# Kernel tuning notes

Hardware: AMD Instinct MI355X
Metric: run time of the kernel (lower is better)

Reference implementation:

```python
import jax, jax.numpy as jnp
import numpy as np

B, C, H_RES, W_RES = 8, 192, 64, 64


def dwconv(x, kern, pad):
    # depthwise conv, x: (B,C,H,W), kern: (C,1,k,k)
    return jax.lax.conv_general_dilated(
        x, kern, window_strides=(1, 1), padding=[(pad, pad), (pad, pad)],
        dimension_numbers=('NCHW', 'OIHW', 'NCHW'),
        feature_group_count=x.shape[1])


def omni_shift(x, alpha, dw1, dw3, dw5):
    # OmniShift (training branch): learnable mix of identity + depthwise 1x1/3x3/5x5
    return (alpha[0] * x + alpha[1] * dwconv(x, dw1, 0)
            + alpha[2] * dwconv(x, dw3, 1) + alpha[3] * dwconv(x, dw5, 2))


def biwkv(w, u, k, v):
    # Bidirectional WKV (Vision-RWKV style):
    # out_t = (sum_{i!=t} e^{-(|t-i|-1)w + k_i} v_i + e^{u+k_t} v_t)
    #       / (sum_{i!=t} e^{-(|t-i|-1)w + k_i}       + e^{u+k_t})
    # w,u: (C,); k,v: (B,T,C). Implemented as two stable log-scaled scans.
    kT = jnp.moveaxis(k, 1, 0)  # (T,B,C)
    vT = jnp.moveaxis(v, 1, 0)
    bc = (k.shape[0], k.shape[2])
    init = (jnp.full(bc, -jnp.inf, k.dtype), jnp.zeros(bc, k.dtype), jnp.zeros(bc, k.dtype))

    def step(carry, inp):
        p, num, den = carry          # state = e^p * (num, den) over strictly-previous tokens
        kt, vt = inp
        out = (p, num, den)          # emit BEFORE absorbing token t (i != t term)
        q = jnp.maximum(p - w, kt)
        e1 = jnp.exp(p - w - q)
        e2 = jnp.exp(kt - q)
        return (q, e1 * num + e2 * vt, e1 * den + e2), out

    _, (pf, nf, df) = jax.lax.scan(step, init, (kT, vT))
    _, (pb, nb, db) = jax.lax.scan(step, init, (kT[::-1], vT[::-1]))
    pb, nb, db = pb[::-1], nb[::-1], db[::-1]

    ps = u + kT                      # self term exponent
    r = jnp.maximum(jnp.maximum(pf, pb), ps)
    ef, eb, es = jnp.exp(pf - r), jnp.exp(pb - r), jnp.exp(ps - r)
    out = (ef * nf + eb * nb + es * vT) / (ef * df + eb * db + es)
    return jnp.moveaxis(out, 0, 1)   # (B,T,C)


def setup_inputs() -> dict:
    key = jax.random.key(0)
    ks = jax.random.split(key, 12)
    s = 1.0 / np.sqrt(C)
    inp = {
        'x': jax.random.normal(ks[0], (B, C, H_RES, W_RES), jnp.float32),
        'w_key': jax.random.normal(ks[1], (C, C), jnp.float32) * s,
        'w_value': jax.random.normal(ks[2], (C, C), jnp.float32) * s,
        'w_recept': jax.random.normal(ks[3], (C, C), jnp.float32) * s,
        'w_out': jax.random.normal(ks[4], (C, C), jnp.float32) * s,
        'decay': jax.random.normal(ks[5], (C,), jnp.float32),
        'boost': jax.random.normal(ks[6], (C,), jnp.float32),
        'alpha': jax.random.normal(ks[7], (4,), jnp.float32),
        'dw1': jax.random.normal(ks[8], (C, 1, 1, 1), jnp.float32) * s,
        'dw3': jax.random.normal(ks[9], (C, 1, 3, 3), jnp.float32) * (s / 3.0),
        'dw5': jax.random.normal(ks[10], (C, 1, 5, 5), jnp.float32) * (s / 5.0),
        'H': H_RES,
        'W': W_RES,
    }
    return inp


def reference(x, w_key, w_value, w_recept, w_out, decay, boost, alpha, dw1, dw3, dw5, H, W):
    Bn, Cn = x.shape[0], x.shape[1]
    T = H * W
    xs = omni_shift(x, alpha, dw1, dw3, dw5)                 # (B,C,H,W)
    xt = jnp.transpose(xs.reshape(Bn, Cn, T), (0, 2, 1))     # (B,T,C)
    k = jnp.einsum('btc,dc->btd', xt, w_key)
    v = jnp.einsum('btc,dc->btd', xt, w_value)
    sr = jax.nn.sigmoid(jnp.einsum('btc,dc->btd', xt, w_recept))
    y = biwkv(decay / T, boost / T, k, v)                    # (B,T,C)
    y = sr * y
    y = jnp.einsum('btd,cd->btc', y, w_out)
    return jnp.transpose(y, (0, 2, 1)).reshape(Bn, Cn, H, W)
```

## Files before the change

kernel.cpp:

```cpp
#include <hip/hip_runtime.h>
#include <math.h>

#define Cn 192
#define Bn 8
#define Tn 4096
#define HW 64

typedef unsigned short u16;
typedef unsigned int u32;
typedef __attribute__((ext_vector_type(8))) __bf16 bf16x8;
typedef __attribute__((ext_vector_type(16))) float f32x16;

__device__ __forceinline__ void gload16(const void* g, void* l) {
    __builtin_amdgcn_global_load_lds(
        (const __attribute__((address_space(1))) void*)g,
        (__attribute__((address_space(3))) void*)l, 16, 0, 0);
}

__device__ __forceinline__ void split_bf16(float x, u16 &h, u16 &l) {
    u32 u = __float_as_uint(x);
    u32 uh = (u + 0x7FFFu + ((u >> 16) & 1u)) & 0xFFFF0000u;
    h = (u16)(uh >> 16);
    float r = x - __uint_as_float(uh);
    u32 ur = __float_as_uint(r);
    l = (u16)((ur + 0x7FFFu + ((ur >> 16) & 1u)) >> 16);
}

__global__ __launch_bounds__(256) void wsplit_kernel(const float* __restrict__ Wk,
                                                     const float* __restrict__ Wv,
                                                     const float* __restrict__ Wr,
                                                     const float* __restrict__ Wo,
                                                     u16* __restrict__ wh,
                                                     u16* __restrict__ wl) {
    const int idx = blockIdx.x * 256 + threadIdx.x;
    const int mat = blockIdx.y;
    const float* src = (mat == 0) ? Wk : (mat == 1) ? Wv : (mat == 2) ? Wr : Wo;
    u16 h, l;
    split_bf16(src[idx], h, l);
    wh[(size_t)mat * 36864 + idx] = h;
    wl[(size_t)mat * 36864 + idx] = l;
}

__global__ __launch_bounds__(256) void omni_kernel(const float* __restrict__ x,
                                                   const float* __restrict__ alpha,
                                                   const float* __restrict__ dw1,
                                                   const float* __restrict__ dw3,
                                                   const float* __restrict__ dw5,
                                                   u16* __restrict__ xhi,
                                                   u16* __restrict__ xlo) {
    const int plane = blockIdx.x;
    const int c = plane % Cn;
    const float* xin = x + (size_t)plane * Tn;
    u16* oh = xhi + (size_t)plane * Tn;
    u16* ol = xlo + (size_t)plane * Tn;

    __shared__ float tile[68 * 68];
    __shared__ float wk[25];

    const int tid = threadIdx.x;
    if (tid == 0) {
        const float a0 = alpha[0], a1 = alpha[1], a2 = alpha[2], a3 = alpha[3];
        #pragma unroll
        for (int j = 0; j < 25; ++j) wk[j] = a3 * dw5[c * 25 + j];
        #pragma unroll
        for (int dy = 0; dy < 3; ++dy)
            #pragma unroll
            for (int dx = 0; dx < 3; ++dx)
                wk[(dy + 1) * 5 + (dx + 1)] += a2 * dw3[c * 9 + dy * 3 + dx];
        wk[12] += a1 * dw1[c] + a0;
    }
    for (int i = tid; i < 68 * 68; i += 256) {
        int r = i / 68, cc = i - r * 68;
        int gy = r - 2, gx = cc - 2;
        float v = 0.f;
        if (gy >= 0 && gy < HW && gx >= 0 && gx < HW) v = xin[gy * HW + gx];
        tile[i] = v;
    }
    __syncthreads();

    const int py = tid >> 3;
    const int px0 = (tid & 7) << 3;

    #pragma unroll
    for (int half = 0; half < 2; ++half) {
        const int y = py + half * 32;
        float row[5][12];
        #pragma unroll
        for (int dy = 0; dy < 5; ++dy) {
            const float4* rp = (const float4*)&tile[(y + dy) * 68 + px0];
            float4 r0 = rp[0], r1 = rp[1], r2 = rp[2];
            row[dy][0] = r0.x; row[dy][1] = r0.y; row[dy][2]  = r0.z; row[dy][3]  = r0.w;
            row[dy][4] = r1.x; row[dy][5] = r1.y; row[dy][6]  = r1.z; row[dy][7]  = r1.w;
            row[dy][8] = r2.x; row[dy][9] = r2.y; row[dy][10] = r2.z; row[dy][11] = r2.w;
        }
        u32 ph[4], pl[4];
        #pragma unroll
        for (int jj = 0; jj < 8; ++jj) {
            float acc = 0.f;
            #pragma unroll
            for (int dy = 0; dy < 5; ++dy)
                #pragma unroll
                for (int dx = 0; dx < 5; ++dx)
                    acc = fmaf(row[dy][jj + dx], wk[dy * 5 + dx], acc);
            u16 h, l2;
            split_bf16(acc, h, l2);
            if (jj & 1) { ph[jj >> 1] |= ((u32)h) << 16; pl[jj >> 1] |= ((u32)l2) << 16; }
            else        { ph[jj >> 1] = h;               pl[jj >> 1] = l2; }
        }
        *(uint4*)&oh[y * 64 + px0] = make_uint4(ph[0], ph[1], ph[2], ph[3]);
        *(uint4*)&ol[y * 64 + px0] = make_uint4(pl[0], pl[1], pl[2], pl[3]);
    }
}

__global__ __launch_bounds__(256) void transpose_kernel(const u16* __restrict__ ih,
                                                        const u16* __restrict__ il,
                                                        u16* __restrict__ oh,
                                                        u16* __restrict__ ol) {
    __shared__ u32 T[2][128][21];
    const int tid = threadIdx.x;
    const size_t ib = (size_t)blockIdx.z * Cn * Tn;
    const int c0 = blockIdx.y * 32, t0 = blockIdx.x * 128;

    {
        const int c2 = tid >> 4;
        const int tc = (tid & 15) * 8;
        const size_t ge = ib + (size_t)(c0 + 2 * c2) * Tn + t0 + tc;
        uint4 evh = *(const uint4*)&ih[ge];
        uint4 odh = *(const uint4*)&ih[ge + Tn];
        uint4 evl = *(const uint4*)&il[ge];
        uint4 odl = *(const uint4*)&il[ge + Tn];
        const u32 eh4[4] = {evh.x, evh.y, evh.z, evh.w};
        const u32 oh4[4] = {odh.x, odh.y, odh.z, odh.w};
        const u32 el4[4] = {evl.x, evl.y, evl.z, evl.w};
        const u32 ol4[4] = {odl.x, odl.y, odl.z, odl.w};
        #pragma unroll
        for (int q = 0; q < 4; ++q) {
            T[0][tc + 2 * q    ][c2] = (eh4[q] & 0xFFFFu) | (oh4[q] << 16);
            T[0][tc + 2 * q + 1][c2] = (eh4[q] >> 16) | (oh4[q] & 0xFFFF0000u);
            T[1][tc + 2 * q    ][c2] = (el4[q] & 0xFFFFu) | (ol4[q] << 16);
            T[1][tc + 2 * q + 1][c2] = (el4[q] >> 16) | (ol4[q] & 0xFFFF0000u);
        }
    }
    __syncthreads();
    {
        const int t = tid >> 1;
        const int hf = tid & 1;
        u32 wv[8][2];
        #pragma unroll
        for (int q = 0; q < 8; ++q) {
            wv[q][0] = T[0][t][hf * 8 + q];
            wv[q][1] = T[1][t][hf * 8 + q];
        }
        const size_t go = ib + (size_t)(t0 + t) * Cn + c0 + hf * 16;
        *(uint4*)&oh[go]     = make_uint4(wv[0][0], wv[1][0], wv[2][0], wv[3][0]);
        *(uint4*)&oh[go + 8] = make_uint4(wv[4][0], wv[5][0], wv[6][0], wv[7][0]);
        *(uint4*)&ol[go]     = make_uint4(wv[0][1], wv[1][1], wv[2][1], wv[3][1]);
        *(uint4*)&ol[go + 8] = make_uint4(wv[4][1], wv[5][1], wv[6][1], wv[7][1]);
    }
}

template<int NM>
__global__ __launch_bounds__(256) void gemm_mfma(const u16* __restrict__ wh,
                                                 const u16* __restrict__ wl,
                                                 const u16* __restrict__ Xh,
                                                 const u16* __restrict__ Xl,
                                                 float* __restrict__ O0,
                                                 float* __restrict__ O1,
                                                 float* __restrict__ O2,
                                                 int wrow0) {
    constexpr int AR  = NM * 64;
    constexpr int ASZ = AR * 32;
    constexpr int BSZ = 128 * 32;
    constexpr int BUF = 2 * ASZ + 2 * BSZ;
    __shared__ u16 lds[2][BUF];

    const int tid  = threadIdx.x;
    const int l    = tid & 63;
    const int wave = tid >> 6;
    const int wm   = wave >> 1, wn = wave & 1;
    const int m0   = blockIdx.y * 64;
    const int t0   = blockIdx.x * 128;
    const size_t xb = (size_t)blockIdx.z * Cn * Tn;

    f32x16 acc[NM][2];
    #pragma unroll
    for (int m = 0; m < NM; ++m)
        #pragma unroll
        for (int nf = 0; nf < 2; ++nf)
            #pragma unroll
            for (int r = 0; r < 16; ++r) acc[m][nf][r] = 0.f;

    auto stage = [&](int bf, int k0) {
        u16* Ah = &lds[bf][0];
        u16* Al = &lds[bf][ASZ];
        u16* Bh = &lds[bf][2 * ASZ];
        u16* Bl = &lds[bf][2 * ASZ + BSZ];
        #pragma unroll
        for (int i = 0; i < NM; ++i) {
            int idx = i * 256 + tid;
            int row = idx >> 2;
            int cb  = (idx & 3) ^ ((row >> 1) & 3);
            int grow = wrow0 + (row >> 6) * 192 + m0 + (row & 63);
            int dst = (i * 256 + wave * 64) * 8;
            gload16(wh + (size_t)grow * Cn + k0 + cb * 8, Ah + dst);
            gload16(wl + (size_t)grow * Cn + k0 + cb * 8, Al + dst);
        }
        #pragma unroll
        for (int i = 0; i < 2; ++i) {
            int idx = i * 256 + tid;
            int tr  = idx >> 2;
            int cb  = (idx & 3) ^ ((tr >> 1) & 3);
            int dst = (i * 256 + wave * 64) * 8;
            gload16(Xh + xb + (size_t)(t0 + tr) * Cn + k0 + cb * 8, Bh + dst);
            gload16(Xl + xb + (size_t)(t0 + tr) * Cn + k0 + cb * 8, Bl + dst);
        }
    };

    auto compute = [&](int bf) {
        const u16* Ah = &lds[bf][0];
        const u16* Al = &lds[bf][ASZ];
        const u16* Bh = &lds[bf][2 * ASZ];
        const u16* Bl = &lds[bf][2 * ASZ + BSZ];
        #pragma unroll
        for (int kh = 0; kh < 2; ++kh) {
            const int cbb = kh * 2 + (l >> 5);
            bf16x8 ah[NM], al[NM];
            #pragma unroll
            for (int m = 0; m < NM; ++m) {
                int r = m * 64 + wm * 32 + (l & 31);
                int off = r * 32 + ((cbb ^ ((r >> 1) & 3)) << 3);
                ah[m] = *(const bf16x8*)&Ah[off];
                al[m] = *(const bf16x8*)&Al[off];
            }
            #pragma unroll
            for (int nf = 0; nf < 2; ++nf) {
                int tr = wn * 64 + nf * 32 + (l & 31);
                int off = tr * 32 + ((cbb ^ ((tr >> 1) & 3)) << 3);
                bf16x8 bh = *(const bf16x8*)&Bh[off];
                bf16x8 bl = *(const bf16x8*)&Bl[off];
                #pragma unroll
                for (int m = 0; m < NM; ++m) {
                    acc[m][nf] = __builtin_amdgcn_mfma_f32_32x32x16_bf16(ah[m], bh, acc[m][nf], 0, 0, 0);
                    acc[m][nf] = __builtin_amdgcn_mfma_f32_32x32x16_bf16(ah[m], bl, acc[m][nf], 0, 0, 0);
                    acc[m][nf] = __builtin_amdgcn_mfma_f32_32x32x16_bf16(al[m], bh, acc[m][nf], 0, 0, 0);
                }
            }
        }
    };

    stage(0, 0);
    __syncthreads();
    for (int ks = 0; ks < 6; ++ks) {
        if (ks < 5) stage((ks + 1) & 1, (ks + 1) * 32);
        compute(ks & 1);
        __syncthreads();
    }

    float* Os[3] = {O0, O1, O2};
    #pragma unroll
    for (int m = 0; m < NM; ++m) {
        float* O = Os[m] + (size_t)blockIdx.z * Cn * Tn;
        #pragma unroll
        for (int nf = 0; nf < 2; ++nf) {
            int col = t0 + wn * 64 + nf * 32 + (l & 31);
            #pragma unroll
            for (int r = 0; r < 16; ++r) {
                int row = m0 + wm * 32 + (r & 3) + 8 * (r >> 2) + 4 * (l >> 5);
                O[(size_t)row * Tn + col] = acc[m][nf][r];
            }
        }
    }
}

__global__ __launch_bounds__(256) void wkv_kernel(const float* __restrict__ kg,
                                                  const float* __restrict__ vg,
                                                  const float* __restrict__ srlg,
                                                  const float* __restrict__ decay,
                                                  const float* __restrict__ boost,
                                                  u16* __restrict__ yhi,
                                                  u16* __restrict__ ylo) {
    const int row = blockIdx.x;
    const int d = row % Cn;
    const float* kr = kg + (size_t)row * Tn;
    const float* vr = vg + (size_t)row * Tn;
    const float* sr = srlg + (size_t)row * Tn;
    u16* yh = yhi + (size_t)row * Tn;
    u16* yl = ylo + (size_t)row * Tn;

    const int tid = threadIdx.x;
    const int t0 = tid * 16;

    float kk[16], vv[16];
    #pragma unroll
    for (int j = 0; j < 16; j += 4) {
        *(float4*)&kk[j] = *(const float4*)&kr[t0 + j];
        *(float4*)&vv[j] = *(const float4*)&vr[t0 + j];
    }

    __shared__ float red[256];
    float lm = kk[0];
    #pragma unroll
    for (int j = 1; j < 16; ++j) lm = fmaxf(lm, kk[j]);
    red[tid] = lm;
    __syncthreads();
    for (int s = 128; s > 0; s >>= 1) {
        if (tid < s) red[tid] = fmaxf(red[tid], red[tid + s]);
        __syncthreads();
    }
    const float m = red[0];
    __syncthreads();

    const float ww = decay[d] * (1.0f / (float)Tn);
    const float u = boost[d] * (1.0f / (float)Tn);
    const float lam = expf(-ww);
    const float lam16 = expf(-16.0f * ww);

    float a[16];
    #pragma unroll
    for (int j = 0; j < 16; ++j) a[j] = expf(kk[j] - m);

    float SN = 0.f, SD = 0.f;
    #pragma unroll
    for (int j = 0; j < 16; ++j) { SN = fmaf(lam, SN, a[j] * vv[j]); SD = fmaf(lam, SD, a[j]); }
    float BN = 0.f, BD = 0.f;
    #pragma unroll
    for (int j = 15; j >= 0; --j) { BN = fmaf(lam, BN, a[j] * vv[j]); BD = fmaf(lam, BD, a[j]); }

    __shared__ float sN[2][256], sD[2][256];

    sN[0][tid] = SN; sD[0][tid] = SD;
    __syncthreads();
    int src = 0;
    float f = lam16;
    for (int o = 1; o < 256; o <<= 1) {
        float nN = sN[src][tid], nD = sD[src][tid];
        if (tid >= o) { nN = fmaf(f, sN[src][tid - o], nN); nD = fmaf(f, sD[src][tid - o], nD); }
        sN[src ^ 1][tid] = nN; sD[src ^ 1][tid] = nD;
        __syncthreads();
        src ^= 1; f = f * f;
    }
    const float CfN = (tid > 0) ? sN[src][tid - 1] : 0.f;
    const float CfD = (tid > 0) ? sD[src][tid - 1] : 0.f;
    __syncthreads();

    sN[0][tid] = BN; sD[0][tid] = BD;
    __syncthreads();
    src = 0; f = lam16;
    for (int o = 1; o < 256; o <<= 1) {
        float nN = sN[src][tid], nD = sD[src][tid];
        if (tid + o < 256) { nN = fmaf(f, sN[src][tid + o], nN); nD = fmaf(f, sD[src][tid + o], nD); }
        sN[src ^ 1][tid] = nN; sD[src ^ 1][tid] = nD;
        __syncthreads();
        src ^= 1; f = f * f;
    }
    const float CbN = (tid < 255) ? sN[src][tid + 1] : 0.f;
    const float CbD = (tid < 255) ? sD[src][tid + 1] : 0.f;

    float fN[16], fD[16];
    float cN = CfN, cD = CfD;
    #pragma unroll
    for (int j = 0; j < 16; ++j) {
        fN[j] = cN; fD[j] = cD;
        cN = fmaf(lam, cN, a[j] * vv[j]);
        cD = fmaf(lam, cD, a[j]);
    }

    float sl[16];
    #pragma unroll
    for (int j = 0; j < 16; j += 4) *(float4*)&sl[j] = *(const float4*)&sr[t0 + j];

    u16 oh[16], ol[16];
    float bN = CbN, bD = CbD;
    #pragma unroll
    for (int j = 15; j >= 0; --j) {
        const float es = expf(u + kk[j] - m);
        const float num = fN[j] + bN + es * vv[j];
        const float den = fD[j] + bD + es;
        const float y = num / den;
        const float sig = 1.0f / (1.0f + expf(-sl[j]));
        split_bf16(sig * y, oh[j], ol[j]);
        bN = fmaf(lam, bN, a[j] * vv[j]);
        bD = fmaf(lam, bD, a[j]);
    }

    u32 ph[8], pl[8];
    #pragma unroll
    for (int j = 0; j < 8; ++j) {
        ph[j] = (u32)oh[2 * j] | ((u32)oh[2 * j + 1] << 16);
        pl[j] = (u32)ol[2 * j] | ((u32)ol[2 * j + 1] << 16);
    }
    *(uint4*)&yh[t0]     = make_uint4(ph[0], ph[1], ph[2], ph[3]);
    *(uint4*)&yh[t0 + 8] = make_uint4(ph[4], ph[5], ph[6], ph[7]);
    *(uint4*)&yl[t0]     = make_uint4(pl[0], pl[1], pl[2], pl[3]);
    *(uint4*)&yl[t0 + 8] = make_uint4(pl[4], pl[5], pl[6], pl[7]);
}

extern "C" void kernel_launch(void* const* d_in, const int* in_sizes, int n_in,
                              void* d_out, int out_size, void* d_ws, size_t ws_size,
                              hipStream_t stream) {
    const float* x        = (const float*)d_in[0];
    const float* w_key    = (const float*)d_in[1];
    const float* w_value  = (const float*)d_in[2];
    const float* w_recept = (const float*)d_in[3];
    const float* w_out    = (const float*)d_in[4];
    const float* decay    = (const float*)d_in[5];
    const float* boost    = (const float*)d_in[6];
    const float* alpha    = (const float*)d_in[7];
    const float* dw1      = (const float*)d_in[8];
    const float* dw3      = (const float*)d_in[9];
    const float* dw5      = (const float*)d_in[10];

    const size_t S = (size_t)Bn * Cn * Tn;
    u16* R0 = (u16*)d_ws;
    u16* R1 = R0 + 2 * S;
    u16* R2 = R1 + 2 * S;
    u16* whp = R2 + 2 * S;
    u16* wlp = whp + 4 * 36864;

    u16* xs_hi = R0;        u16* xs_lo = R0 + S;
    u16* Xt_hi = R1;        u16* Xt_lo = R1 + S;
    float* kb  = (float*)R0;
    float* vb  = (float*)R2;
    float* srl = (float*)d_out;
    u16* y_hi  = R1;        u16* y_lo  = R1 + S;
    u16* Yt_hi = R2;        u16* Yt_lo = R2 + S;
    float* out = (float*)d_out;

    wsplit_kernel<<<dim3(144, 4), 256, 0, stream>>>(w_key, w_value, w_recept, w_out, whp, wlp);

    omni_kernel<<<dim3(Bn * Cn), 256, 0, stream>>>(x, alpha, dw1, dw3, dw5, xs_hi, xs_lo);

    transpose_kernel<<<dim3(32, 6, 8), 256, 0, stream>>>(xs_hi, xs_lo, Xt_hi, Xt_lo);

    gemm_mfma<3><<<dim3(32, 3, 8), 256, 0, stream>>>(whp, wlp, Xt_hi, Xt_lo, kb, vb, srl, 0);

    wkv_kernel<<<dim3(Bn * Cn), 256, 0, stream>>>(kb, vb, srl, decay, boost, y_hi, y_lo);

    transpose_kernel<<<dim3(32, 6, 8), 256, 0, stream>>>(y_hi, y_lo, Yt_hi, Yt_lo);

    gemm_mfma<1><<<dim3(32, 3, 8), 256, 0, stream>>>(whp, wlp, Yt_hi, Yt_lo, out, nullptr, nullptr, 576);
}
```

Measured before the change: 122.8 us.

## Fold weight split into transpose launch and single-buffer A tile in GEMM

Removes the separate weight-splitting kernel by giving the first transpose launch an extra z-slice of blocks that does the bf16 hi/lo split of all four weight matrices. This saves one launch. In the GEMM, the weight (A) tile is now single-buffered while the activation (B) tile stays double-buffered, which cuts LDS use and may allow more resident blocks. The cost is an extra barrier per k-step, and the A load is no longer overlapped with compute.

```diff
diff --git a/kernel.cpp b/kernel.cpp
--- a/kernel.cpp
+++ b/kernel.cpp
@@ -24,21 +24,6 @@
     float r = x - __uint_as_float(uh);
     u32 ur = __float_as_uint(r);
     l = (u16)((ur + 0x7FFFu + ((ur >> 16) & 1u)) >> 16);
-}
-
-__global__ __launch_bounds__(256) void wsplit_kernel(const float* __restrict__ Wk,
-                                                     const float* __restrict__ Wv,
-                                                     const float* __restrict__ Wr,
-                                                     const float* __restrict__ Wo,
-                                                     u16* __restrict__ wh,
-                                                     u16* __restrict__ wl) {
-    const int idx = blockIdx.x * 256 + threadIdx.x;
-    const int mat = blockIdx.y;
-    const float* src = (mat == 0) ? Wk : (mat == 1) ? Wv : (mat == 2) ? Wr : Wo;
-    u16 h, l;
-    split_bf16(src[idx], h, l);
-    wh[(size_t)mat * 36864 + idx] = h;
-    wl[(size_t)mat * 36864 + idx] = l;
 }
 
 __global__ __launch_bounds__(256) void omni_kernel(const float* __restrict__ x,
@@ -115,9 +100,31 @@
 __global__ __launch_bounds__(256) void transpose_kernel(const u16* __restrict__ ih,
                                                         const u16* __restrict__ il,
                                                         u16* __restrict__ oh,
-                                                        u16* __restrict__ ol) {
+                                                        u16* __restrict__ ol,
+                                                        const float* __restrict__ Wk,
+                                                        const float* __restrict__ Wv,
+                                                        const float* __restrict__ Wr,
+                                                        const float* __restrict__ Wo,
+                                                        u16* __restrict__ wh,
+                                                        u16* __restrict__ wl) {
+    const int tid = threadIdx.x;
+    if (blockIdx.z == 8) {
+        const int base = (blockIdx.y * 32 + blockIdx.x) * 768;
+        #pragma unroll
+        for (int j = 0; j < 3; ++j) {
+            int idx = base + j * 256 + tid;
+            int mat = idx / 36864;
+            int off = idx - mat * 36864;
+            const float* src = (mat == 0) ? Wk : (mat == 1) ? Wv : (mat == 2) ? Wr : Wo;
+            u16 h, l;
+            split_bf16(src[off], h, l);
+            wh[idx] = h;
+            wl[idx] = l;
+        }
+        return;
+    }
+
     __shared__ u32 T[2][128][21];
-    const int tid = threadIdx.x;
     const size_t ib = (size_t)blockIdx.z * Cn * Tn;
     const int c0 = blockIdx.y * 32, t0 = blockIdx.x * 128;
 
@@ -168,11 +175,10 @@
                                                  float* __restrict__ O1,
                                                  float* __restrict__ O2,
                                                  int wrow0) {
-    constexpr int AR  = NM * 64;
-    constexpr int ASZ = AR * 32;
+    constexpr int ASZ = NM * 64 * 32;
     constexpr int BSZ = 128 * 32;
-    constexpr int BUF = 2 * ASZ + 2 * BSZ;
-    __shared__ u16 lds[2][BUF];
+    __shared__ u16 A_[2 * ASZ];
+    __shared__ u16 B_[2][2 * BSZ];
 
     const int tid  = threadIdx.x;
     const int l    = tid & 63;
@@ -190,11 +196,7 @@
             #pragma unroll
             for (int r = 0; r < 16; ++r) acc[m][nf][r] = 0.f;
 
-    auto stage = [&](int bf, int k0) {
-        u16* Ah = &lds[bf][0];
-        u16* Al = &lds[bf][ASZ];
-        u16* Bh = &lds[bf][2 * ASZ];
-        u16* Bl = &lds[bf][2 * ASZ + BSZ];
+    auto stageA = [&](int k0) {
         #pragma unroll
         for (int i = 0; i < NM; ++i) {
             int idx = i * 256 + tid;
@@ -202,25 +204,26 @@
             int cb  = (idx & 3) ^ ((row >> 1) & 3);
             int grow = wrow0 + (row >> 6) * 192 + m0 + (row & 63);
             int dst = (i * 256 + wave * 64) * 8;
-            gload16(wh + (size_t)grow * Cn + k0 + cb * 8, Ah + dst);
-            gload16(wl + (size_t)grow * Cn + k0 + cb * 8, Al + dst);
-        }
+            gload16(wh + (size_t)grow * Cn + k0 + cb * 8, A_ + dst);
+            gload16(wl + (size_t)grow * Cn + k0 + cb * 8, A_ + ASZ + dst);
+        }
+    };
+    auto stageB = [&](int bf, int k0) {
         #pragma unroll
         for (int i = 0; i < 2; ++i) {
             int idx = i * 256 + tid;
             int tr  = idx >> 2;
             int cb  = (idx & 3) ^ ((tr >> 1) & 3);
             int dst = (i * 256 + wave * 64) * 8;
-            gload16(Xh + xb + (size_t)(t0 + tr) * Cn + k0 + cb * 8, Bh + dst);
-            gload16(Xl + xb + (size_t)(t0 + tr) * Cn + k0 + cb * 8, Bl + dst);
+            gload16(Xh + xb + (size_t)(t0 + tr) * Cn + k0 + cb * 8, B_[bf] + dst);
+            gload16(Xl + xb + (size_t)(t0 + tr) * Cn + k0 + cb * 8, B_[bf] + BSZ + dst);
         }
     };
-
     auto compute = [&](int bf) {
-        const u16* Ah = &lds[bf][0];
-        const u16* Al = &lds[bf][ASZ];
-        const u16* Bh = &lds[bf][2 * ASZ];
-        const u16* Bl = &lds[bf][2 * ASZ + BSZ];
+        const u16* Ah = A_;
+        const u16* Al = A_ + ASZ;
+        const u16* Bh = B_[bf];
+        const u16* Bl = B_[bf] + BSZ;
         #pragma unroll
         for (int kh = 0; kh < 2; ++kh) {
             const int cbb = kh * 2 + (l >> 5);
@@ -248,12 +251,17 @@
         }
     };
 
-    stage(0, 0);
+    stageA(0);
+    stageB(0, 0);
     __syncthreads();
     for (int ks = 0; ks < 6; ++ks) {
-        if (ks < 5) stage((ks + 1) & 1, (ks + 1) * 32);
+        if (ks < 5) stageB((ks + 1) & 1, (ks + 1) * 32);
         compute(ks & 1);
         __syncthreads();
+        if (ks < 5) {
+            stageA((ks + 1) * 32);
+            __syncthreads();
+        }
     }
 
     float* Os[3] = {O0, O1, O2};
@@ -426,17 +434,19 @@
     u16* Yt_hi = R2;        u16* Yt_lo = R2 + S;
     float* out = (float*)d_out;
 
-    wsplit_kernel<<<dim3(144, 4), 256, 0, stream>>>(w_key, w_value, w_recept, w_out, whp, wlp);
-
     omni_kernel<<<dim3(Bn * Cn), 256, 0, stream>>>(x, alpha, dw1, dw3, dw5, xs_hi, xs_lo);
 
-    transpose_kernel<<<dim3(32, 6, 8), 256, 0, stream>>>(xs_hi, xs_lo, Xt_hi, Xt_lo);
+    transpose_kernel<<<dim3(32, 6, 9), 256, 0, stream>>>(xs_hi, xs_lo, Xt_hi, Xt_lo,
+                                                         w_key, w_value, w_recept, w_out,
+                                                         whp, wlp);
 
     gemm_mfma<3><<<dim3(32, 3, 8), 256, 0, stream>>>(whp, wlp, Xt_hi, Xt_lo, kb, vb, srl, 0);
 
     wkv_kernel<<<dim3(Bn * Cn), 256, 0, stream>>>(kb, vb, srl, decay, boost, y_hi, y_lo);
 
-    transpose_kernel<<<dim3(32, 6, 8), 256, 0, stream>>>(y_hi, y_lo, Yt_hi, Yt_lo);
+    transpose_kernel<<<dim3(32, 6, 8), 256, 0, stream>>>(y_hi, y_lo, Yt_hi, Yt_lo,
+                                                         w_key, w_value, w_recept, w_out,
+                                                         whp, wlp);
 
     gemm_mfma<1><<<dim3(32, 3, 8), 256, 0, stream>>>(whp, wlp, Yt_hi, Yt_lo, out, nullptr, nullptr, 576);
 }
```

Result: faster. 119.2 us (-3.0%).
